# Optimization experiments

Measured on AMD Instinct MI355X. Metric: run time of the kernel, lower is better.

The kernel has to match this reference:

```python
import jax, jax.numpy as jnp
import numpy as np

H = 1024
NH = 16
DH = 64
FF = 2 * H
EPS = 1e-6


def setup_inputs() -> dict:
    key = jax.random.key(0)
    ks = jax.random.split(key, 16)
    s = 0.02
    inp = {
        'x': jax.random.normal(ks[0], (4, 1024, H), jnp.float32),
        'y': jax.random.normal(ks[1], (4, 2048, H), jnp.float32),
        'Wq': jax.random.normal(ks[2], (H, H), jnp.float32) * s,
        'bq': jnp.zeros((H,), jnp.float32),
        'Wk': jax.random.normal(ks[3], (H, H), jnp.float32) * s,
        'bk': jnp.zeros((H,), jnp.float32),
        'Wv': jax.random.normal(ks[4], (H, H), jnp.float32) * s,
        'bv': jnp.zeros((H,), jnp.float32),
        'Wm': jax.random.normal(ks[5], (H, H), jnp.float32) * s,
        'bm': jnp.zeros((H,), jnp.float32),
        'W1': jax.random.normal(ks[6], (H, FF), jnp.float32) * s,
        'b1': jnp.zeros((FF,), jnp.float32),
        'W2': jax.random.normal(ks[7], (FF, H), jnp.float32) * s,
        'b2': jnp.zeros((H,), jnp.float32),
        'g1': jnp.ones((H,), jnp.float32),
        'be1': jnp.zeros((H,), jnp.float32),
        'g2': jnp.ones((H,), jnp.float32),
        'be2': jnp.zeros((H,), jnp.float32),
    }
    return inp


def _layernorm(x, g, b):
    # torch: a_2 * (x - mean) / (std + eps) + b_2, std unbiased (ddof=1)
    mean = jnp.mean(x, axis=-1, keepdims=True)
    std = jnp.std(x, axis=-1, keepdims=True, ddof=1)
    return g * (x - mean) / (std + EPS) + b


def reference(x, y, Wq, bq, Wk, bk, Wv, bv, Wm, bm, W1, b1, W2, b2, g1, be1, g2, be2):
    B, Lq, _ = x.shape
    Lk = y.shape[1]
    # QKV projections + split heads: [B, L, NH, DH]
    q = (x @ Wq + bq).reshape(B, Lq, NH, DH)
    k = (y @ Wk + bk).reshape(B, Lk, NH, DH)
    v = (y @ Wv + bv).reshape(B, Lk, NH, DH)
    # sigmoid attention (no softmax / no row normalization)
    scores = jnp.einsum('bqhd,bkhd->bhqk', q, k) / jnp.sqrt(jnp.float32(DH))
    att_map = jax.nn.sigmoid(scores)  # [B, NH, Lq, Lk]
    atted = jnp.einsum('bhqk,bkhd->bqhd', att_map, v).reshape(B, Lq, H)
    atted = atted @ Wm + bm
    # residual + custom LayerNorm, FFN, residual + LayerNorm
    h = _layernorm(x + atted, g1, be1)
    ffn = jax.nn.relu(h @ W1 + b1) @ W2 + b2
    out = _layernorm(h + ffn, g2, be2)
    return out, att_map
```

## Files before the change

kernel.cpp:

```cpp
#include <hip/hip_runtime.h>
#include <hip/hip_bf16.h>

typedef __attribute__((ext_vector_type(8))) __bf16 bf16x8;
typedef __attribute__((ext_vector_type(4))) float f32x4;

__device__ inline unsigned short f2bf(float f) {
  unsigned int u = __float_as_uint(f);
  u += 0x7fffu + ((u >> 16) & 1u);
  return (unsigned short)(u >> 16);
}

__device__ inline void glds16(const void* g, void* l) {
  __builtin_amdgcn_global_load_lds((const __attribute__((address_space(1))) void*)g,
                                   (__attribute__((address_space(3))) void*)l,
                                   16, 0, 0);
}

__global__ __launch_bounds__(256) void cast_kernel(const float* __restrict__ in,
                                                   unsigned short* __restrict__ out,
                                                   int n4) {
  int i = blockIdx.x * 256 + threadIdx.x;
  if (i >= n4) return;
  float4 v = ((const float4*)in)[i];
  ushort4 o;
  o.x = f2bf(v.x); o.y = f2bf(v.y); o.z = f2bf(v.z); o.w = f2bf(v.w);
  ((ushort4*)out)[i] = o;
}

__global__ __launch_bounds__(256) void transpose_cast(const float* __restrict__ in,
                                                      unsigned short* __restrict__ out,
                                                      int R, int C) {
  __shared__ float tile[32][33];
  int tx = threadIdx.x & 31, ty = threadIdx.x >> 5;
  int c = blockIdx.x * 32 + tx;
#pragma unroll
  for (int k = 0; k < 4; ++k) {
    int r = blockIdx.y * 32 + ty + k * 8;
    tile[ty + k * 8][tx] = in[(size_t)r * C + c];
  }
  __syncthreads();
  int rr = blockIdx.y * 32 + tx;
#pragma unroll
  for (int k = 0; k < 4; ++k) {
    int cc = blockIdx.x * 32 + ty + k * 8;
    out[(size_t)cc * R + rr] = f2bf(tile[tx][ty + k * 8]);
  }
}

template <int MODE>
__global__ __launch_bounds__(256) void gemm_bt(
    const unsigned short* __restrict__ A, const unsigned short* __restrict__ Bt,
    int M, int N, int K,
    const float* __restrict__ bias,
    float* __restrict__ outf, unsigned short* __restrict__ outb,
    const float* __restrict__ resid, int lshift, int L) {
  __shared__ __attribute__((aligned(16))) unsigned short As[128 * 32];
  __shared__ __attribute__((aligned(16))) unsigned short Bs[64 * 32];
  const int tid = threadIdx.x;
  const int l = tid & 63;
  const int lr = l & 15, lc = l >> 4;
  const int w = tid >> 6;
  const int wrow = (w >> 1) << 6;
  const int wcol = (w & 1) << 5;
  const long bm0 = (long)blockIdx.x * 128;
  const long bn0 = (long)blockIdx.y * 64;

  f32x4 acc[4][2];
#pragma unroll
  for (int m = 0; m < 4; ++m)
#pragma unroll
    for (int n = 0; n < 2; ++n) acc[m][n] = f32x4{0.f, 0.f, 0.f, 0.f};

  const int r0 = tid >> 2, p0 = tid & 3;
  const int c1 = tid + 256;
  const int r1 = c1 >> 2, p1 = c1 & 3;
  const unsigned short* a0 = A + (bm0 + r0) * K + ((p0 ^ ((r0 >> 1) & 3)) << 3);
  const unsigned short* a1 = A + (bm0 + r1) * K + ((p1 ^ ((r1 >> 1) & 3)) << 3);
  const unsigned short* b0 = Bt + (bn0 + r0) * K + ((p0 ^ ((r0 >> 1) & 3)) << 3);

  for (int k0 = 0; k0 < K; k0 += 32) {
    glds16(a0 + k0, &As[tid * 8]);
    glds16(a1 + k0, &As[c1 * 8]);
    glds16(b0 + k0, &Bs[tid * 8]);
    __syncthreads();
    bf16x8 a[4], b[2];
#pragma unroll
    for (int m = 0; m < 4; ++m) {
      int row = wrow + m * 16 + lr;
      a[m] = *(const bf16x8*)&As[row * 32 + ((lc ^ ((row >> 1) & 3)) << 3)];
    }
#pragma unroll
    for (int n = 0; n < 2; ++n) {
      int row = wcol + n * 16 + lr;
      b[n] = *(const bf16x8*)&Bs[row * 32 + ((lc ^ ((row >> 1) & 3)) << 3)];
    }
#pragma unroll
    for (int m = 0; m < 4; ++m)
#pragma unroll
      for (int n = 0; n < 2; ++n)
        acc[m][n] = __builtin_amdgcn_mfma_f32_16x16x32_bf16(a[m], b[n], acc[m][n], 0, 0, 0);
    __syncthreads();
  }

#pragma unroll
  for (int m = 0; m < 4; ++m)
#pragma unroll
    for (int n = 0; n < 2; ++n)
#pragma unroll
      for (int r = 0; r < 4; ++r) {
        const int gm = (int)bm0 + wrow + m * 16 + lc * 4 + r;
        const int gn = (int)bn0 + wcol + n * 16 + lr;
        float val = acc[m][n][r] + bias[gn];
        if constexpr (MODE == 0) {
          const int bb = gm >> lshift, rl = gm & (L - 1);
          const int hh = gn >> 6, dd = gn & 63;
          outb[((((size_t)bb * 16 + hh) * L + rl) << 6) + dd] = f2bf(val);
        } else if constexpr (MODE == 1) {
          const int bb = gm >> lshift, rl = gm & (L - 1);
          const int hh = gn >> 6, dd = gn & 63;
          outb[(((size_t)bb * 16 + hh) * 64 + dd) * L + rl] = f2bf(val);
        } else if constexpr (MODE == 2) {
          const size_t idx = (size_t)gm * N + gn;
          outf[idx] = val + resid[idx];
        } else {
          outb[(size_t)gm * N + gn] = f2bf(fmaxf(val, 0.f));
        }
      }
}

__global__ __launch_bounds__(256) void attn_kernel(
    const unsigned short* __restrict__ qb, const unsigned short* __restrict__ kb,
    const unsigned short* __restrict__ vtb,
    float* __restrict__ amap_out, unsigned short* __restrict__ atted) {
  constexpr int Lq = 1024, Lk = 2048, DH = 64, NH = 16;
  constexpr int PS = 152;
  __shared__ __attribute__((aligned(16))) unsigned short Qs[128 * 64];
  __shared__ __attribute__((aligned(16))) unsigned short KVs[128 * 64];
  __shared__ __attribute__((aligned(16))) unsigned short Ps[128 * PS];
  const int tid = threadIdx.x;
  const int l = tid & 63, w = tid >> 6;
  const int lr = l & 15, lc = l >> 4;
  const int wr = (w >> 1) * 64;
  const int wc = (w & 1) * 64;
  const int pwc = (w & 1) * 32;
  const int qt = blockIdx.x, h = blockIdx.y, b = blockIdx.z;
  const unsigned short* qhead = qb + ((size_t)(b * NH + h) * Lq + qt * 128) * DH;
  const unsigned short* khead = kb + (size_t)(b * NH + h) * Lk * DH;
  const unsigned short* vhead = vtb + (size_t)(b * NH + h) * DH * Lk;
  float* amap = amap_out + ((size_t)(b * NH + h) * Lq + qt * 128) * Lk;

#pragma unroll
  for (int i = 0; i < 4; ++i) {
    int c = i * 256 + tid;
    int row = c >> 3, p = c & 7;
    glds16(qhead + row * DH + ((p ^ (row & 7)) << 3), &Qs[c * 8]);
  }

  f32x4 pacc[4][2];
#pragma unroll
  for (int m = 0; m < 4; ++m)
#pragma unroll
    for (int n = 0; n < 2; ++n) pacc[m][n] = f32x4{0.f, 0.f, 0.f, 0.f};

  for (int kt = 0; kt < 16; ++kt) {
    const unsigned short* ksrc = khead + (size_t)kt * 128 * DH;
#pragma unroll
    for (int i = 0; i < 4; ++i) {
      int c = i * 256 + tid;
      int row = c >> 3, p = c & 7;
      glds16(ksrc + row * DH + ((p ^ (row & 7)) << 3), &KVs[c * 8]);
    }
    __syncthreads();

    f32x4 sacc[4][4];
#pragma unroll
    for (int m = 0; m < 4; ++m)
#pragma unroll
      for (int n = 0; n < 4; ++n) sacc[m][n] = f32x4{0.f, 0.f, 0.f, 0.f};
    bf16x8 aq[4][2], bk[4][2];
#pragma unroll
    for (int m = 0; m < 4; ++m)
#pragma unroll
      for (int s = 0; s < 2; ++s) {
        int row = wr + m * 16 + lr;
        int g = s * 4 + lc;
        aq[m][s] = *(const bf16x8*)&Qs[row * 64 + ((g ^ (row & 7)) << 3)];
      }
#pragma unroll
    for (int n = 0; n < 4; ++n)
#pragma unroll
      for (int s = 0; s < 2; ++s) {
        int row = wc + n * 16 + lr;
        int g = s * 4 + lc;
        bk[n][s] = *(const bf16x8*)&KVs[row * 64 + ((g ^ (row & 7)) << 3)];
      }
#pragma unroll
    for (int m = 0; m < 4; ++m)
#pragma unroll
      for (int n = 0; n < 4; ++n)
#pragma unroll
        for (int s = 0; s < 2; ++s)
          sacc[m][n] = __builtin_amdgcn_mfma_f32_16x16x32_bf16(aq[m][s], bk[n][s], sacc[m][n], 0, 0, 0);

    float* amap_t = amap + kt * 128;
#pragma unroll
    for (int m = 0; m < 4; ++m)
#pragma unroll
      for (int n = 0; n < 4; ++n)
#pragma unroll
        for (int r = 0; r < 4; ++r) {
          int qrow = wr + m * 16 + lc * 4 + r;
          int kcol = wc + n * 16 + lr;
          float att = 1.0f / (1.0f + __expf(-0.125f * sacc[m][n][r]));
          amap_t[(size_t)qrow * Lk + kcol] = att;
          Ps[qrow * PS + kcol] = f2bf(att);
        }
    __syncthreads();

    const unsigned short* vsrc = vhead + kt * 128;
#pragma unroll
    for (int i = 0; i < 4; ++i) {
      int c = i * 256 + tid;
      int d = c >> 4, p = c & 15;
      glds16(vsrc + (size_t)d * Lk + ((p ^ (d & 15)) << 3), &KVs[c * 8]);
    }
    __syncthreads();

    bf16x8 pa[4][4], pb[2][4];
#pragma unroll
    for (int m = 0; m < 4; ++m)
#pragma unroll
      for (int s = 0; s < 4; ++s)
        pa[m][s] = *(const bf16x8*)&Ps[(wr + m * 16 + lr) * PS + s * 32 + lc * 8];
#pragma unroll
    for (int n = 0; n < 2; ++n)
#pragma unroll
      for (int s = 0; s < 4; ++s) {
        int d = pwc + n * 16 + lr;
        int g = s * 4 + lc;
        pb[n][s] = *(const bf16x8*)&KVs[d * 128 + ((g ^ (d & 15)) << 3)];
      }
#pragma unroll
    for (int m = 0; m < 4; ++m)
#pragma unroll
      for (int n = 0; n < 2; ++n)
#pragma unroll
        for (int s = 0; s < 4; ++s)
          pacc[m][n] = __builtin_amdgcn_mfma_f32_16x16x32_bf16(pa[m][s], pb[n][s], pacc[m][n], 0, 0, 0);
    __syncthreads();
  }

#pragma unroll
  for (int m = 0; m < 4; ++m)
#pragma unroll
    for (int n = 0; n < 2; ++n)
#pragma unroll
      for (int r = 0; r < 4; ++r) {
        int q = wr + m * 16 + lc * 4 + r;
        int dd = pwc + n * 16 + lr;
        atted[(size_t)(b * Lq + qt * 128 + q) * 1024 + h * 64 + dd] = f2bf(pacc[m][n][r]);
      }
}

__global__ __launch_bounds__(256) void ln_kernel(
    const float* __restrict__ in, const float* __restrict__ gw,
    const float* __restrict__ bw, float* __restrict__ outf,
    unsigned short* __restrict__ outb) {
  __shared__ float red[8];
  const int row = blockIdx.x, tid = threadIdx.x;
  const float4 v = ((const float4*)(in + (size_t)row * 1024))[tid];
  float s = v.x + v.y + v.z + v.w;
#pragma unroll
  for (int o = 32; o >= 1; o >>= 1) s += __shfl_down(s, o, 64);
  if ((tid & 63) == 0) red[tid >> 6] = s;
  __syncthreads();
  const float mean = (red[0] + red[1] + red[2] + red[3]) * (1.0f / 1024.0f);
  const float dx = v.x - mean, dy = v.y - mean, dz = v.z - mean, dw = v.w - mean;
  float sq = dx * dx + dy * dy + dz * dz + dw * dw;
#pragma unroll
  for (int o = 32; o >= 1; o >>= 1) sq += __shfl_down(sq, o, 64);
  if ((tid & 63) == 0) red[4 + (tid >> 6)] = sq;
  __syncthreads();
  const float var = (red[4] + red[5] + red[6] + red[7]) * (1.0f / 1023.0f);
  const float inv = 1.0f / (sqrtf(var) + 1e-6f);
  const float4 g4 = ((const float4*)gw)[tid];
  const float4 b4 = ((const float4*)bw)[tid];
  float4 o;
  o.x = g4.x * dx * inv + b4.x;
  o.y = g4.y * dy * inv + b4.y;
  o.z = g4.z * dz * inv + b4.z;
  o.w = g4.w * dw * inv + b4.w;
  ((float4*)(outf + (size_t)row * 1024))[tid] = o;
  if (outb) {
    ushort4 ob;
    ob.x = f2bf(o.x); ob.y = f2bf(o.y); ob.z = f2bf(o.z); ob.w = f2bf(o.w);
    *(ushort4*)(outb + (size_t)row * 1024 + tid * 4) = ob;
  }
}

extern "C" void kernel_launch(void* const* d_in, const int* in_sizes, int n_in,
                              void* d_out, int out_size, void* d_ws, size_t ws_size,
                              hipStream_t stream) {
  const float* x  = (const float*)d_in[0];
  const float* y  = (const float*)d_in[1];
  const float* Wq = (const float*)d_in[2];
  const float* bq = (const float*)d_in[3];
  const float* Wk = (const float*)d_in[4];
  const float* bk = (const float*)d_in[5];
  const float* Wv = (const float*)d_in[6];
  const float* bv = (const float*)d_in[7];
  const float* Wm = (const float*)d_in[8];
  const float* bm = (const float*)d_in[9];
  const float* W1 = (const float*)d_in[10];
  const float* b1 = (const float*)d_in[11];
  const float* W2 = (const float*)d_in[12];
  const float* b2 = (const float*)d_in[13];
  const float* g1 = (const float*)d_in[14];
  const float* be1 = (const float*)d_in[15];
  const float* g2 = (const float*)d_in[16];
  const float* be2 = (const float*)d_in[17];

  float* out = (float*)d_out;
  float* amap = out + (size_t)4 * 1024 * 1024;

  char* ws = (char*)d_ws;
  unsigned short* xb  = (unsigned short*)(ws);
  unsigned short* yb  = (unsigned short*)(ws + 8388608);
  unsigned short* Wqt = (unsigned short*)(ws + 25165824);
  unsigned short* Wkt = Wqt + 1024 * 1024;
  unsigned short* Wvt = Wkt + 1024 * 1024;
  unsigned short* Wmt = Wvt + 1024 * 1024;
  unsigned short* W1t = Wmt + 1024 * 1024;
  unsigned short* W2t = W1t + 2048 * 1024;
  unsigned short* qb  = (unsigned short*)(ws + 41943040);
  unsigned short* kb  = (unsigned short*)(ws + 50331648);
  unsigned short* vtb = (unsigned short*)(ws + 67108864);
  unsigned short* attedb = (unsigned short*)(ws + 83886080);
  float* h1 = (float*)(ws + 50331648);
  float* hf = (float*)(ws + 67108864);
  unsigned short* hb = (unsigned short*)(ws);
  unsigned short* ffnb = (unsigned short*)(ws + 8388608);
  float* h2 = (float*)(ws + 50331648);

  cast_kernel<<<4096, 256, 0, stream>>>(x, xb, 1024 * 1024);
  cast_kernel<<<8192, 256, 0, stream>>>(y, yb, 2 * 1024 * 1024);
  transpose_cast<<<dim3(32, 32), 256, 0, stream>>>(Wq, Wqt, 1024, 1024);
  transpose_cast<<<dim3(32, 32), 256, 0, stream>>>(Wk, Wkt, 1024, 1024);
  transpose_cast<<<dim3(32, 32), 256, 0, stream>>>(Wv, Wvt, 1024, 1024);
  transpose_cast<<<dim3(32, 32), 256, 0, stream>>>(Wm, Wmt, 1024, 1024);
  transpose_cast<<<dim3(64, 32), 256, 0, stream>>>(W1, W1t, 1024, 2048);
  transpose_cast<<<dim3(32, 64), 256, 0, stream>>>(W2, W2t, 2048, 1024);

  gemm_bt<0><<<dim3(32, 16), 256, 0, stream>>>(xb, Wqt, 4096, 1024, 1024, bq, nullptr, qb,  nullptr, 10, 1024);
  gemm_bt<0><<<dim3(64, 16), 256, 0, stream>>>(yb, Wkt, 8192, 1024, 1024, bk, nullptr, kb,  nullptr, 11, 2048);
  gemm_bt<1><<<dim3(64, 16), 256, 0, stream>>>(yb, Wvt, 8192, 1024, 1024, bv, nullptr, vtb, nullptr, 11, 2048);

  attn_kernel<<<dim3(8, 16, 4), 256, 0, stream>>>(qb, kb, vtb, amap, attedb);

  gemm_bt<2><<<dim3(32, 16), 256, 0, stream>>>(attedb, Wmt, 4096, 1024, 1024, bm, h1, nullptr, x, 0, 0);
  ln_kernel<<<4096, 256, 0, stream>>>(h1, g1, be1, hf, hb);
  gemm_bt<3><<<dim3(32, 32), 256, 0, stream>>>(hb, W1t, 4096, 2048, 1024, b1, nullptr, ffnb, nullptr, 0, 0);
  gemm_bt<2><<<dim3(32, 16), 256, 0, stream>>>(ffnb, W2t, 4096, 1024, 2048, b2, h2, nullptr, hf, 0, 0);
  ln_kernel<<<4096, 256, 0, stream>>>(h2, g2, be2, out, nullptr);
}
```

Baseline: 975.5 us.

## Enlarge GEMM tiles to 128x128, stage V-transpose via LDS, keep Q in registers

The GEMM block tile grows from 128x64 to 128x128, with each wave computing 64x64, so more MFMAs run per LDS load and the grids shrink to match. The MODE 1 (V transposed) epilogue now writes through an LDS transpose buffer and emits 16-byte vector stores instead of scattered 2-byte stores. The attention kernel loads Q fragments once from global memory into registers instead of staging them in LDS, and reduces the P buffer padding. The trade-off is more accumulator registers, which may lower occupancy, and fewer blocks for the smaller GEMMs.

```diff
diff --git a/kernel.cpp b/kernel.cpp
--- a/kernel.cpp
+++ b/kernel.cpp
@@ -55,74 +55,97 @@
     float* __restrict__ outf, unsigned short* __restrict__ outb,
     const float* __restrict__ resid, int lshift, int L) {
   __shared__ __attribute__((aligned(16))) unsigned short As[128 * 32];
-  __shared__ __attribute__((aligned(16))) unsigned short Bs[64 * 32];
+  __shared__ __attribute__((aligned(16))) unsigned short Bs[128 * 32];
+  __shared__ __attribute__((aligned(16))) unsigned short Tr[(MODE == 1) ? 128 * 136 : 8];
   const int tid = threadIdx.x;
   const int l = tid & 63;
   const int lr = l & 15, lc = l >> 4;
   const int w = tid >> 6;
-  const int wrow = (w >> 1) << 6;
-  const int wcol = (w & 1) << 5;
+  const int wr = (w >> 1) << 6;
+  const int wc = (w & 1) << 6;
   const long bm0 = (long)blockIdx.x * 128;
-  const long bn0 = (long)blockIdx.y * 64;
-
-  f32x4 acc[4][2];
-#pragma unroll
-  for (int m = 0; m < 4; ++m)
-#pragma unroll
-    for (int n = 0; n < 2; ++n) acc[m][n] = f32x4{0.f, 0.f, 0.f, 0.f};
+  const long bn0 = (long)blockIdx.y * 128;
+
+  f32x4 acc[4][4];
+#pragma unroll
+  for (int m = 0; m < 4; ++m)
+#pragma unroll
+    for (int n = 0; n < 4; ++n) acc[m][n] = f32x4{0.f, 0.f, 0.f, 0.f};
 
   const int r0 = tid >> 2, p0 = tid & 3;
-  const int c1 = tid + 256;
-  const int r1 = c1 >> 2, p1 = c1 & 3;
-  const unsigned short* a0 = A + (bm0 + r0) * K + ((p0 ^ ((r0 >> 1) & 3)) << 3);
-  const unsigned short* a1 = A + (bm0 + r1) * K + ((p1 ^ ((r1 >> 1) & 3)) << 3);
-  const unsigned short* b0 = Bt + (bn0 + r0) * K + ((p0 ^ ((r0 >> 1) & 3)) << 3);
+  const int swz = p0 ^ ((r0 >> 1) & 3);
+  const unsigned short* a0 = A + (bm0 + r0) * K + (swz << 3);
+  const unsigned short* b0 = Bt + (bn0 + r0) * K + (swz << 3);
 
   for (int k0 = 0; k0 < K; k0 += 32) {
     glds16(a0 + k0, &As[tid * 8]);
-    glds16(a1 + k0, &As[c1 * 8]);
+    glds16(a0 + 64 * K + k0, &As[(256 + tid) * 8]);
     glds16(b0 + k0, &Bs[tid * 8]);
-    __syncthreads();
-    bf16x8 a[4], b[2];
+    glds16(b0 + 64 * K + k0, &Bs[(256 + tid) * 8]);
+    __syncthreads();
+    bf16x8 a[4], b[4];
 #pragma unroll
     for (int m = 0; m < 4; ++m) {
-      int row = wrow + m * 16 + lr;
+      int row = wr + m * 16 + lr;
       a[m] = *(const bf16x8*)&As[row * 32 + ((lc ^ ((row >> 1) & 3)) << 3)];
     }
 #pragma unroll
-    for (int n = 0; n < 2; ++n) {
-      int row = wcol + n * 16 + lr;
+    for (int n = 0; n < 4; ++n) {
+      int row = wc + n * 16 + lr;
       b[n] = *(const bf16x8*)&Bs[row * 32 + ((lc ^ ((row >> 1) & 3)) << 3)];
     }
 #pragma unroll
     for (int m = 0; m < 4; ++m)
 #pragma unroll
-      for (int n = 0; n < 2; ++n)
+      for (int n = 0; n < 4; ++n)
         acc[m][n] = __builtin_amdgcn_mfma_f32_16x16x32_bf16(a[m], b[n], acc[m][n], 0, 0, 0);
     __syncthreads();
   }
 
-#pragma unroll
-  for (int m = 0; m < 4; ++m)
-#pragma unroll
-    for (int n = 0; n < 2; ++n)
+  if constexpr (MODE == 1) {
+#pragma unroll
+    for (int m = 0; m < 4; ++m)
+#pragma unroll
+      for (int n = 0; n < 4; ++n)
+#pragma unroll
+        for (int r = 0; r < 4; ++r) {
+          const int lm = wr + m * 16 + lc * 4 + r;
+          const int ln = wc + n * 16 + lr;
+          Tr[ln * 136 + lm] = f2bf(acc[m][n][r] + bias[bn0 + ln]);
+        }
+    __syncthreads();
+#pragma unroll
+    for (int rep = 0; rep < 8; ++rep) {
+      const int c = rep * 256 + tid;
+      const int ln = c >> 4;
+      const int lm0 = (c & 15) * 8;
+      const bf16x8 vv = *(const bf16x8*)&Tr[ln * 136 + lm0];
+      const int gm = (int)bm0 + lm0;
+      const int gn = (int)bn0 + ln;
+      const int bb = gm >> lshift, rl = gm & (L - 1);
+      const int hh = gn >> 6, dd = gn & 63;
+      *(bf16x8*)&outb[(((size_t)bb * 16 + hh) * 64 + dd) * L + rl] = vv;
+    }
+    return;
+  }
+
+#pragma unroll
+  for (int m = 0; m < 4; ++m)
+#pragma unroll
+    for (int n = 0; n < 4; ++n)
 #pragma unroll
       for (int r = 0; r < 4; ++r) {
-        const int gm = (int)bm0 + wrow + m * 16 + lc * 4 + r;
-        const int gn = (int)bn0 + wcol + n * 16 + lr;
+        const int gm = (int)bm0 + wr + m * 16 + lc * 4 + r;
+        const int gn = (int)bn0 + wc + n * 16 + lr;
         float val = acc[m][n][r] + bias[gn];
         if constexpr (MODE == 0) {
           const int bb = gm >> lshift, rl = gm & (L - 1);
           const int hh = gn >> 6, dd = gn & 63;
           outb[((((size_t)bb * 16 + hh) * L + rl) << 6) + dd] = f2bf(val);
-        } else if constexpr (MODE == 1) {
-          const int bb = gm >> lshift, rl = gm & (L - 1);
-          const int hh = gn >> 6, dd = gn & 63;
-          outb[(((size_t)bb * 16 + hh) * 64 + dd) * L + rl] = f2bf(val);
         } else if constexpr (MODE == 2) {
           const size_t idx = (size_t)gm * N + gn;
           outf[idx] = val + resid[idx];
-        } else {
+        } else if constexpr (MODE == 3) {
           outb[(size_t)gm * N + gn] = f2bf(fmaxf(val, 0.f));
         }
       }
@@ -133,8 +156,7 @@
     const unsigned short* __restrict__ vtb,
     float* __restrict__ amap_out, unsigned short* __restrict__ atted) {
   constexpr int Lq = 1024, Lk = 2048, DH = 64, NH = 16;
-  constexpr int PS = 152;
-  __shared__ __attribute__((aligned(16))) unsigned short Qs[128 * 64];
+  constexpr int PS = 136;
   __shared__ __attribute__((aligned(16))) unsigned short KVs[128 * 64];
   __shared__ __attribute__((aligned(16))) unsigned short Ps[128 * PS];
   const int tid = threadIdx.x;
@@ -149,12 +171,12 @@
   const unsigned short* vhead = vtb + (size_t)(b * NH + h) * DH * Lk;
   float* amap = amap_out + ((size_t)(b * NH + h) * Lq + qt * 128) * Lk;
 
-#pragma unroll
-  for (int i = 0; i < 4; ++i) {
-    int c = i * 256 + tid;
-    int row = c >> 3, p = c & 7;
-    glds16(qhead + row * DH + ((p ^ (row & 7)) << 3), &Qs[c * 8]);
-  }
+  bf16x8 aq[4][2];
+#pragma unroll
+  for (int m = 0; m < 4; ++m)
+#pragma unroll
+    for (int s = 0; s < 2; ++s)
+      aq[m][s] = *(const bf16x8*)&qhead[(wr + m * 16 + lr) * DH + (s * 4 + lc) * 8];
 
   f32x4 pacc[4][2];
 #pragma unroll
@@ -177,15 +199,7 @@
     for (int m = 0; m < 4; ++m)
 #pragma unroll
       for (int n = 0; n < 4; ++n) sacc[m][n] = f32x4{0.f, 0.f, 0.f, 0.f};
-    bf16x8 aq[4][2], bk[4][2];
-#pragma unroll
-    for (int m = 0; m < 4; ++m)
-#pragma unroll
-      for (int s = 0; s < 2; ++s) {
-        int row = wr + m * 16 + lr;
-        int g = s * 4 + lc;
-        aq[m][s] = *(const bf16x8*)&Qs[row * 64 + ((g ^ (row & 7)) << 3)];
-      }
+    bf16x8 bk[4][2];
 #pragma unroll
     for (int n = 0; n < 4; ++n)
 #pragma unroll
@@ -351,15 +365,15 @@
   transpose_cast<<<dim3(64, 32), 256, 0, stream>>>(W1, W1t, 1024, 2048);
   transpose_cast<<<dim3(32, 64), 256, 0, stream>>>(W2, W2t, 2048, 1024);
 
-  gemm_bt<0><<<dim3(32, 16), 256, 0, stream>>>(xb, Wqt, 4096, 1024, 1024, bq, nullptr, qb,  nullptr, 10, 1024);
-  gemm_bt<0><<<dim3(64, 16), 256, 0, stream>>>(yb, Wkt, 8192, 1024, 1024, bk, nullptr, kb,  nullptr, 11, 2048);
-  gemm_bt<1><<<dim3(64, 16), 256, 0, stream>>>(yb, Wvt, 8192, 1024, 1024, bv, nullptr, vtb, nullptr, 11, 2048);
+  gemm_bt<0><<<dim3(32, 8), 256, 0, stream>>>(xb, Wqt, 4096, 1024, 1024, bq, nullptr, qb,  nullptr, 10, 1024);
+  gemm_bt<0><<<dim3(64, 8), 256, 0, stream>>>(yb, Wkt, 8192, 1024, 1024, bk, nullptr, kb,  nullptr, 11, 2048);
+  gemm_bt<1><<<dim3(64, 8), 256, 0, stream>>>(yb, Wvt, 8192, 1024, 1024, bv, nullptr, vtb, nullptr, 11, 2048);
 
   attn_kernel<<<dim3(8, 16, 4), 256, 0, stream>>>(qb, kb, vtb, amap, attedb);
 
-  gemm_bt<2><<<dim3(32, 16), 256, 0, stream>>>(attedb, Wmt, 4096, 1024, 1024, bm, h1, nullptr, x, 0, 0);
+  gemm_bt<2><<<dim3(32, 8), 256, 0, stream>>>(attedb, Wmt, 4096, 1024, 1024, bm, h1, nullptr, x, 0, 0);
   ln_kernel<<<4096, 256, 0, stream>>>(h1, g1, be1, hf, hb);
-  gemm_bt<3><<<dim3(32, 32), 256, 0, stream>>>(hb, W1t, 4096, 2048, 1024, b1, nullptr, ffnb, nullptr, 0, 0);
-  gemm_bt<2><<<dim3(32, 16), 256, 0, stream>>>(ffnb, W2t, 4096, 1024, 2048, b2, h2, nullptr, hf, 0, 0);
+  gemm_bt<3><<<dim3(32, 16), 256, 0, stream>>>(hb, W1t, 4096, 2048, 1024, b1, nullptr, ffnb, nullptr, 0, 0);
+  gemm_bt<2><<<dim3(32, 8), 256, 0, stream>>>(ffnb, W2t, 4096, 1024, 2048, b2, h2, nullptr, hf, 0, 0);
   ln_kernel<<<4096, 256, 0, stream>>>(h2, g2, be2, out, nullptr);
 }
```

Result: no change. 989.6 us (+1.4%).
